# Performance work log

Measured on AMD Instinct MI355X. Metric: run time of the kernel, lower is better.

The kernel has to match this reference:

```python
import jax, jax.numpy as jnp
import numpy as np

N_FACES = 40000
N_EDGES = 60000
NNZ = 3 * N_FACES  # 3 boundary edges per triangular face
IN_CH = 512
MID_CH = 512
OUT_CH = 512


def setup_inputs() -> dict:
    key = jax.random.key(0)
    k1, k2, k3 = jax.random.split(key, 3)
    x = jax.random.normal(k1, (N_FACES, IN_CH), dtype=jnp.float32)
    # xavier-uniform-ish scale with gain 1.414 as in TopoModelX Conv.reset_parameters
    W1 = jax.random.normal(k2, (IN_CH, MID_CH), dtype=jnp.float32) * (1.414 / np.sqrt(IN_CH))
    W2 = jax.random.normal(k3, (MID_CH, OUT_CH), dtype=jnp.float32) * (1.414 / np.sqrt(MID_CH))
    # COO incidence B2 [n_edges, n_faces]: face f -> edges (3f)%E,(3f+1)%E,(3f+2)%E
    i = jnp.arange(NNZ)
    face_idx = (i // 3).astype(jnp.int32)
    edge_idx = (i % N_EDGES).astype(jnp.int32)
    vals = jnp.ones((NNZ,), dtype=jnp.float32)
    return {"x": x, "W1": W1, "W2": W2, "edge_idx": edge_idx, "face_idx": face_idx, "vals": vals}


def _spmm(rows, cols, vals, x, n_rows):
    # y[r, :] = sum_{nnz with row r} vals * x[col, :]
    return jax.ops.segment_sum(vals[:, None] * x[cols], rows, num_segments=n_rows)


def reference(x, W1, W2, edge_idx, face_idx, vals):
    # row sums of B2 and B2^T for aggr_norm
    deg_e = jax.ops.segment_sum(vals, edge_idx, num_segments=N_EDGES)  # [n_edges]
    deg_f = jax.ops.segment_sum(vals, face_idx, num_segments=N_FACES)  # [n_faces]
    # conv level1: faces -> edges
    h = _spmm(edge_idx, face_idx, vals, x @ W1, N_EDGES)  # [n_edges, mid]
    h = jax.nn.sigmoid(h / deg_e[:, None])
    # conv level2: edges -> faces (transpose incidence)
    y = _spmm(face_idx, edge_idx, vals, h @ W2, N_FACES)  # [n_faces, out]
    return jax.nn.sigmoid(y / deg_f[:, None])
```

## Files before the change

kernel.cpp:

```cpp
#include <hip/hip_runtime.h>
#include <cstdint>

#define N_FACES_C 40000
#define N_EDGES_C 60000
#define CH        512

typedef __bf16 bf16_t;
typedef __bf16 bf16x8 __attribute__((ext_vector_type(8)));
typedef float  f32x4  __attribute__((ext_vector_type(4)));
static_assert(sizeof(bf16x8) == 16, "bf16x8 must be 16B");

__global__ void detect_dtype(const unsigned int* __restrict__ vals_bits, int* __restrict__ flag) {
  if (blockIdx.x == 0 && threadIdx.x == 0)
    *flag = (vals_bits[0] == 0x3F803F80u) ? 1 : 0;
}

__device__ __forceinline__ float load_val(const void* vals, int i, bool isbf16) {
  return isbf16 ? (float)((const bf16_t*)vals)[i] : ((const float*)vals)[i];
}

__device__ __forceinline__ float fast_sigmoid(float z) {
  float e = __builtin_amdgcn_exp2f(z * -1.44269504f);
  return __builtin_amdgcn_rcpf(1.0f + e);
}

__device__ __forceinline__ void swz_block(int gx, int gy, int& obx, int& oby) {
  int orig = blockIdx.y * gx + blockIdx.x;
  int nwg = gx * gy;
  int q = nwg >> 3, r = nwg & 7;
  int xcd = orig & 7, idx = orig >> 3;
  int wg = (xcd < r ? xcd * (q + 1) : r * (q + 1) + (xcd - r) * q) + idx;
  obx = wg % gx;
  oby = wg / gx;
}

__global__ void count_deg_kernel(const int* __restrict__ ei, const int* __restrict__ fi,
                                 const void* __restrict__ vals, int nnz,
                                 float* __restrict__ deg_e, float* __restrict__ deg_f,
                                 int* __restrict__ cnt_e, int* __restrict__ cnt_f,
                                 const int* __restrict__ flag) {
  int i = blockIdx.x * 256 + threadIdx.x;
  if (i >= nnz) return;
  bool isb = (*flag != 0);
  float v = load_val(vals, i, isb);
  int e = ei[i], f = fi[i];
  atomicAdd(&deg_e[e], v);
  atomicAdd(&deg_f[f], v);
  atomicAdd(&cnt_e[e], 1);
  atomicAdd(&cnt_f[f], 1);
}

__global__ void scan_part2(const int* __restrict__ cntE, int nE, int* __restrict__ bsumE,
                           const int* __restrict__ cntF, int nF, int* __restrict__ bsumF,
                           int nbE) {
  __shared__ int wsum[4];
  int bx = blockIdx.x;
  const int* cnt; int n; int* bsum; int b;
  if (bx < nbE) { cnt = cntE; n = nE; bsum = bsumE; b = bx; }
  else          { cnt = cntF; n = nF; bsum = bsumF; b = bx - nbE; }
  int t = threadIdx.x;
  int lane = t & 63, wave = t >> 6;
  int base = b * 1024 + t * 4;
  int s = 0;
#pragma unroll
  for (int k = 0; k < 4; ++k) {
    int idx = base + k;
    if (idx < n) s += cnt[idx];
  }
#pragma unroll
  for (int o = 32; o > 0; o >>= 1) s += __shfl_down(s, o);
  if (lane == 0) wsum[wave] = s;
  __syncthreads();
  if (t == 0) bsum[b] = wsum[0] + wsum[1] + wsum[2] + wsum[3];
}

__global__ void scan_bsums2(int* __restrict__ bsumE, int nbE, int* __restrict__ bsumF, int nbF) {
  int wave = threadIdx.x >> 6;
  int lane = threadIdx.x & 63;
  int* bsum = wave ? bsumF : bsumE;
  int nb    = wave ? nbF   : nbE;
  int orig = (lane < nb) ? bsum[lane] : 0;
  int v = orig;
#pragma unroll
  for (int o = 1; o < 64; o <<= 1) {
    int u = __shfl_up(v, o);
    if (lane >= o) v += u;
  }
  if (lane < nb) bsum[lane] = v - orig;
}

__global__ void scan_final2(const int* __restrict__ cntE, int nE, const int* __restrict__ bsumE,
                            int* __restrict__ ptrE, int* __restrict__ curE,
                            const int* __restrict__ cntF, int nF, const int* __restrict__ bsumF,
                            int* __restrict__ ptrF, int* __restrict__ curF, int nbE) {
  __shared__ int wsum[4];
  int bx = blockIdx.x;
  const int* cnt; int n; const int* bsum; int* ptr; int* cur; int b;
  if (bx < nbE) { cnt = cntE; n = nE; bsum = bsumE; ptr = ptrE; cur = curE; b = bx; }
  else          { cnt = cntF; n = nF; bsum = bsumF; ptr = ptrF; cur = curF; b = bx - nbE; }
  int t = threadIdx.x;
  int lane = t & 63, wave = t >> 6;
  int base = b * 1024 + t * 4;
  int c[4];
  int s = 0;
#pragma unroll
  for (int k = 0; k < 4; ++k) {
    int idx = base + k;
    c[k] = (idx < n) ? cnt[idx] : 0;
    s += c[k];
  }
  int v = s;
#pragma unroll
  for (int o = 1; o < 64; o <<= 1) {
    int u = __shfl_up(v, o);
    if (lane >= o) v += u;
  }
  if (lane == 63) wsum[wave] = v;
  __syncthreads();
  int woff = 0;
  for (int w = 0; w < wave; ++w) woff += wsum[w];
  int run = bsum[b] + woff + (v - s);
#pragma unroll
  for (int k = 0; k < 4; ++k) {
    int idx = base + k;
    if (idx < n) {
      ptr[idx] = run;
      cur[idx] = run;
      run += c[k];
      if (idx == n - 1) ptr[n] = run;
    }
  }
}

__global__ void csr_fill(const int* __restrict__ ei, const int* __restrict__ fi,
                         const void* __restrict__ vals, int nnz,
                         int* __restrict__ cur_e, int* __restrict__ col_e, float* __restrict__ val_e,
                         int* __restrict__ cur_f, int* __restrict__ col_f, float* __restrict__ val_f,
                         const int* __restrict__ flag) {
  int i = blockIdx.x * 256 + threadIdx.x;
  if (i >= nnz) return;
  bool isb = (*flag != 0);
  int e = ei[i], f = fi[i];
  float v = load_val(vals, i, isb);
  int p = atomicAdd(&cur_e[e], 1);
  col_e[p] = f; val_e[p] = v;
  int q = atomicAdd(&cur_f[f], 1);
  col_f[q] = e; val_f[q] = v;
}

__global__ void transposeW2(const void* __restrict__ W1, bf16_t* __restrict__ W1t,
                            const void* __restrict__ W2, bf16_t* __restrict__ W2t,
                            const int* __restrict__ flag) {
  __shared__ bf16_t tile[32][33];
  bool isb = (*flag != 0);
  const void* W = blockIdx.z ? W2 : W1;
  bf16_t*    Wt = blockIdx.z ? W2t : W1t;
  int bx = blockIdx.x * 32, by = blockIdx.y * 32;
  int tx = threadIdx.x, ty = threadIdx.y;
#pragma unroll
  for (int r = 0; r < 32; r += 8) {
    size_t idx = (size_t)(by + ty + r) * CH + bx + tx;
    tile[ty + r][tx] = isb ? ((const bf16_t*)W)[idx] : (bf16_t)((const float*)W)[idx];
  }
  __syncthreads();
#pragma unroll
  for (int r = 0; r < 32; r += 8)
    Wt[(size_t)(bx + ty + r) * CH + by + tx] = tile[tx][ty + r];
}

template <int SIG>
__global__ void spmm_row(const int* __restrict__ ptr, const int* __restrict__ cols,
                         const float* __restrict__ vals, const bf16_t* __restrict__ X,
                         const float* __restrict__ deg, bf16_t* __restrict__ Y,
                         int nRows, int nCols, int nnz) {
  int row = blockIdx.x * 4 + (threadIdx.x >> 6);
  if (row >= nRows) return;
  int lane = threadIdx.x & 63;
  int beg = ptr[row], end = ptr[row + 1];
  if (beg < 0) beg = 0;
  if (end > nnz) end = nnz;
  float acc[8];
#pragma unroll
  for (int t = 0; t < 8; ++t) acc[t] = 0.f;
  const int lofs = lane * 8;
  for (int p = beg; p < end; ++p) {
    int c = cols[p];
    if ((unsigned)c >= (unsigned)nCols) c = 0;
    float v = vals[p];
    bf16x8 xv = *(const bf16x8*)(X + (size_t)c * CH + lofs);
#pragma unroll
    for (int t = 0; t < 8; ++t) acc[t] += v * (float)xv[t];
  }
  float d = deg[row];
  float invd = (d != 0.f) ? (1.0f / d) : 0.f;
  bf16x8 o;
#pragma unroll
  for (int t = 0; t < 8; ++t) {
    float z = acc[t] * invd;
    o[t] = (bf16_t)(SIG ? fast_sigmoid(z) : z);
  }
  *(bf16x8*)(Y + (size_t)row * CH + lofs) = o;
}

__global__ __launch_bounds__(256)
void gemm_xw(const void* __restrict__ A, const bf16_t* __restrict__ Bt,
             bf16_t* __restrict__ C, int M, const int* __restrict__ flag) {
  __shared__ __align__(16) bf16_t As[128 * 64];
  __shared__ __align__(16) bf16_t Bs[128 * 64];
  const int tid  = threadIdx.x;
  const int lane = tid & 63;
  const int wave = tid >> 6;
  int bx, by;
  swz_block(gridDim.x, gridDim.y, bx, by);
  const int r0 = by * 128;
  const int c0 = bx * 128;
  const int wr = (wave >> 1) * 64;
  const int wc = (wave & 1) * 64;
  const int q   = lane >> 4;
  const int l16 = lane & 15;
  const int srow_base = wave * 8 + (lane >> 3);
  const int sslot = lane & 7;
  const bool ab = (*flag != 0);

  f32x4 acc[4][4];
#pragma unroll
  for (int i = 0; i < 4; ++i)
#pragma unroll
    for (int j = 0; j < 4; ++j)
      acc[i][j] = (f32x4){0.f, 0.f, 0.f, 0.f};

  for (int kt = 0; kt < 8; ++kt) {
    const int kb = kt * 64;
    if (ab) {
      const bf16_t* Ab = (const bf16_t*)A;
#pragma unroll
      for (int i = 0; i < 4; ++i) {
        const int lr = i * 32 + srow_base;
        const int gofs = (sslot ^ (lr & 7)) * 8;
        int ra = r0 + lr; if (ra > M - 1) ra = M - 1;
        __builtin_amdgcn_global_load_lds((const __attribute__((address_space(1))) void*)(Ab + (size_t)ra * CH + kb + gofs),
                                         (__attribute__((address_space(3))) void*)(As + (i * 32 + wave * 8) * 64), 16, 0, 0);
        __builtin_amdgcn_global_load_lds((const __attribute__((address_space(1))) void*)(Bt + (size_t)(c0 + lr) * CH + kb + gofs),
                                         (__attribute__((address_space(3))) void*)(Bs + (i * 32 + wave * 8) * 64), 16, 0, 0);
      }
    } else {
      const float* Af = (const float*)A;
#pragma unroll
      for (int i = 0; i < 4; ++i) {
        const int lr = i * 32 + srow_base;
        const int gofs = (sslot ^ (lr & 7)) * 8;
        int ra = r0 + lr; if (ra > M - 1) ra = M - 1;
        const float* src = Af + (size_t)ra * CH + kb + gofs;
        float4 a = *(const float4*)src;
        float4 b = *(const float4*)(src + 4);
        bf16x8 v;
        v[0] = (bf16_t)a.x; v[1] = (bf16_t)a.y; v[2] = (bf16_t)a.z; v[3] = (bf16_t)a.w;
        v[4] = (bf16_t)b.x; v[5] = (bf16_t)b.y; v[6] = (bf16_t)b.z; v[7] = (bf16_t)b.w;
        *(bf16x8*)(As + lr * 64 + sslot * 8) = v;
        __builtin_amdgcn_global_load_lds((const __attribute__((address_space(1))) void*)(Bt + (size_t)(c0 + lr) * CH + kb + gofs),
                                         (__attribute__((address_space(3))) void*)(Bs + (i * 32 + wave * 8) * 64), 16, 0, 0);
      }
    }
    __syncthreads();

#pragma unroll
    for (int kk = 0; kk < 2; ++kk) {
      const int slot = (kk * 4 + q) ^ (l16 & 7);
      const int ro = slot * 8;
      bf16x8 af[4], bfv[4];
#pragma unroll
      for (int i = 0; i < 4; ++i)
        af[i] = *(const bf16x8*)(As + (wr + i * 16 + l16) * 64 + ro);
#pragma unroll
      for (int j = 0; j < 4; ++j)
        bfv[j] = *(const bf16x8*)(Bs + (wc + j * 16 + l16) * 64 + ro);
#pragma unroll
      for (int i = 0; i < 4; ++i)
#pragma unroll
        for (int j = 0; j < 4; ++j)
          acc[i][j] = __builtin_amdgcn_mfma_f32_16x16x32_bf16(af[i], bfv[j], acc[i][j], 0, 0, 0);
    }
    __syncthreads();
  }

#pragma unroll
  for (int i = 0; i < 4; ++i) {
#pragma unroll
    for (int r = 0; r < 4; ++r) {
      int row = r0 + wr + i * 16 + q * 4 + r;
      if (row < M) {
#pragma unroll
        for (int j = 0; j < 4; ++j) {
          int col = c0 + wc + j * 16 + l16;
          C[(size_t)row * CH + col] = (bf16_t)acc[i][j][r];
        }
      }
    }
  }
}

__global__ __launch_bounds__(256)
void gemm_sig(const bf16_t* __restrict__ A, const bf16_t* __restrict__ Bt,
              void* __restrict__ C, int M,
              const int* __restrict__ flag) {
  __shared__ __align__(16) bf16_t As[128 * 64];
  __shared__ __align__(16) bf16_t Bs[128 * 64];
  const int tid  = threadIdx.x;
  const int lane = tid & 63;
  const int wave = tid >> 6;
  int bx, by;
  swz_block(gridDim.x, gridDim.y, bx, by);
  const int r0 = by * 128;
  const int c0 = bx * 128;
  const int wr = (wave >> 1) * 64;
  const int wc = (wave & 1) * 64;
  const int q   = lane >> 4;
  const int l16 = lane & 15;
  const int srow_base = wave * 8 + (lane >> 3);
  const int sslot = lane & 7;

  f32x4 acc[4][4];
#pragma unroll
  for (int i = 0; i < 4; ++i)
#pragma unroll
    for (int j = 0; j < 4; ++j)
      acc[i][j] = (f32x4){0.f, 0.f, 0.f, 0.f};

  for (int kt = 0; kt < 8; ++kt) {
    const int kb = kt * 64;
#pragma unroll
    for (int i = 0; i < 4; ++i) {
      const int lr = i * 32 + srow_base;
      const int gofs = (sslot ^ (lr & 7)) * 8;
      int ra = r0 + lr; if (ra > M - 1) ra = M - 1;
      const bf16_t* ga = A  + (size_t)ra * CH + kb + gofs;
      const bf16_t* gb = Bt + (size_t)(c0 + lr) * CH + kb + gofs;
      __builtin_amdgcn_global_load_lds((const __attribute__((address_space(1))) void*)ga,
                                       (__attribute__((address_space(3))) void*)(As + (i * 32 + wave * 8) * 64), 16, 0, 0);
      __builtin_amdgcn_global_load_lds((const __attribute__((address_space(1))) void*)gb,
                                       (__attribute__((address_space(3))) void*)(Bs + (i * 32 + wave * 8) * 64), 16, 0, 0);
    }
    __syncthreads();

#pragma unroll
    for (int kk = 0; kk < 2; ++kk) {
      const int slot = (kk * 4 + q) ^ (l16 & 7);
      const int ro = slot * 8;
      bf16x8 af[4], bfv[4];
#pragma unroll
      for (int i = 0; i < 4; ++i)
        af[i] = *(const bf16x8*)(As + (wr + i * 16 + l16) * 64 + ro);
#pragma unroll
      for (int j = 0; j < 4; ++j)
        bfv[j] = *(const bf16x8*)(Bs + (wc + j * 16 + l16) * 64 + ro);
#pragma unroll
      for (int i = 0; i < 4; ++i)
#pragma unroll
        for (int j = 0; j < 4; ++j)
          acc[i][j] = __builtin_amdgcn_mfma_f32_16x16x32_bf16(af[i], bfv[j], acc[i][j], 0, 0, 0);
    }
    __syncthreads();
  }

  const bool f32out = (*flag == 0);
#pragma unroll
  for (int i = 0; i < 4; ++i) {
#pragma unroll
    for (int r = 0; r < 4; ++r) {
      int row = r0 + wr + i * 16 + q * 4 + r;
      if (row < M) {
#pragma unroll
        for (int j = 0; j < 4; ++j) {
          int col = c0 + wc + j * 16 + l16;
          float s = fast_sigmoid(acc[i][j][r]);
          if (f32out) ((float*)C)[(size_t)row * CH + col] = s;
          else        ((bf16_t*)C)[(size_t)row * CH + col] = (bf16_t)s;
        }
      }
    }
  }
}

extern "C" void kernel_launch(void* const* d_in, const int* in_sizes, int n_in,
                              void* d_out, int out_size, void* d_ws, size_t ws_size,
                              hipStream_t stream) {
  const void* x    = d_in[0];
  const void* W1   = d_in[1];
  const void* W2   = d_in[2];
  const int*  ei   = (const int*)d_in[3];
  const int*  fi   = (const int*)d_in[4];
  const void* vals = d_in[5];
  const int nnz = in_sizes[3];

  char* ws = (char*)d_ws;
  size_t off = 0;
  auto alloc = [&](size_t bytes) -> void* {
    void* p = ws + off;
    off = (off + bytes + 511) & ~((size_t)511);
    return p;
  };
  bf16_t* t    = (bf16_t*)alloc((size_t)N_FACES_C * CH * 2);
  bf16_t* h    = (bf16_t*)alloc((size_t)N_EDGES_C * CH * 2);
  bf16_t* g    = (bf16_t*)alloc((size_t)N_FACES_C * CH * 2);
  bf16_t* w1t  = (bf16_t*)alloc((size_t)CH * CH * 2);
  bf16_t* w2t  = (bf16_t*)alloc((size_t)CH * CH * 2);
  float* deg_e = (float*)alloc((size_t)N_EDGES_C * 4);
  float* deg_f = (float*)alloc((size_t)N_FACES_C * 4);
  int*   cnt_e = (int*)alloc((size_t)N_EDGES_C * 4);
  int*   cnt_f = (int*)alloc((size_t)N_FACES_C * 4);
  size_t zero_bytes = (size_t)((char*)cnt_f + (size_t)N_FACES_C * 4 - (char*)deg_e);
  int*   ptr_e = (int*)alloc((size_t)(N_EDGES_C + 1) * 4);
  int*   ptr_f = (int*)alloc((size_t)(N_FACES_C + 1) * 4);
  int*   cur_e = (int*)alloc((size_t)N_EDGES_C * 4);
  int*   cur_f = (int*)alloc((size_t)N_FACES_C * 4);
  int*   col_e = (int*)alloc((size_t)nnz * 4);
  float* val_e = (float*)alloc((size_t)nnz * 4);
  int*   col_f = (int*)alloc((size_t)nnz * 4);
  float* val_f = (float*)alloc((size_t)nnz * 4);
  int*   bsumE = (int*)alloc(64 * 4);
  int*   bsumF = (int*)alloc(64 * 4);
  int*   flag  = (int*)alloc(4);

  detect_dtype<<<1, 64, 0, stream>>>((const unsigned int*)vals, flag);
  hipMemsetAsync(deg_e, 0, zero_bytes, stream);
  count_deg_kernel<<<(nnz + 255) / 256, 256, 0, stream>>>(ei, fi, vals, nnz,
                                                          deg_e, deg_f, cnt_e, cnt_f, flag);

  int nbE = (N_EDGES_C + 1023) / 1024, nbF = (N_FACES_C + 1023) / 1024;
  scan_part2 <<<nbE + nbF, 256, 0, stream>>>(cnt_e, N_EDGES_C, bsumE, cnt_f, N_FACES_C, bsumF, nbE);
  scan_bsums2<<<1, 128, 0, stream>>>(bsumE, nbE, bsumF, nbF);
  scan_final2<<<nbE + nbF, 256, 0, stream>>>(cnt_e, N_EDGES_C, bsumE, ptr_e, cur_e,
                                             cnt_f, N_FACES_C, bsumF, ptr_f, cur_f, nbE);
  csr_fill<<<(nnz + 255) / 256, 256, 0, stream>>>(ei, fi, vals, nnz,
                                                  cur_e, col_e, val_e, cur_f, col_f, val_f, flag);

  transposeW2<<<dim3(16, 16, 2), dim3(32, 8), 0, stream>>>(W1, w1t, W2, w2t, flag);

  gemm_xw<<<dim3(CH / 128, (N_FACES_C + 127) / 128), 256, 0, stream>>>(x, w1t, t, N_FACES_C, flag);
  spmm_row<1><<<(N_EDGES_C + 3) / 4, 256, 0, stream>>>(ptr_e, col_e, val_e, t, deg_e, h,
                                                       N_EDGES_C, N_FACES_C, nnz);
  spmm_row<0><<<(N_FACES_C + 3) / 4, 256, 0, stream>>>(ptr_f, col_f, val_f, h, deg_f, g,
                                                       N_FACES_C, N_EDGES_C, nnz);
  gemm_sig<<<dim3(CH / 128, (N_FACES_C + 127) / 128), 256, 0, stream>>>(g, w2t, d_out,
                                                                        N_FACES_C, flag);
}
```

Measured before the change: 315.0 us.

## Double-buffer LDS tiles in both GEMM kernels to overlap loads with MFMA

Both GEMM kernels now keep two LDS buffers per operand and prefetch the next K-tile while MFMAs run on the current one. One barrier per iteration replaces the previous two. The fp32 input path holds the next tile in registers and converts and stores it after compute. The aim is to hide global-load latency behind matrix math, at the cost of doubled LDS use (64KB per block), which may lower occupancy.

New measurement: 311.3 us. No clear change (-1.2%).

```diff
diff --git a/kernel.cpp b/kernel.cpp
--- a/kernel.cpp
+++ b/kernel.cpp
@@ -202,11 +202,12 @@
   *(bf16x8*)(Y + (size_t)row * CH + lofs) = o;
 }
 
+
 __global__ __launch_bounds__(256)
 void gemm_xw(const void* __restrict__ A, const bf16_t* __restrict__ Bt,
              bf16_t* __restrict__ C, int M, const int* __restrict__ flag) {
-  __shared__ __align__(16) bf16_t As[128 * 64];
-  __shared__ __align__(16) bf16_t Bs[128 * 64];
+  __shared__ __align__(16) bf16_t As[2][128 * 64];
+  __shared__ __align__(16) bf16_t Bs[2][128 * 64];
   const int tid  = threadIdx.x;
   const int lane = tid & 63;
   const int wave = tid >> 6;
@@ -222,6 +223,15 @@
   const int sslot = lane & 7;
   const bool ab = (*flag != 0);
 
+  int lr_[4], gofs_[4], ra_[4];
+#pragma unroll
+  for (int i = 0; i < 4; ++i) {
+    lr_[i] = i * 32 + srow_base;
+    gofs_[i] = (sslot ^ (lr_[i] & 7)) * 8;
+    int ra = r0 + lr_[i]; if (ra > M - 1) ra = M - 1;
+    ra_[i] = ra;
+  }
+
   f32x4 acc[4][4];
 #pragma unroll
   for (int i = 0; i < 4; ++i)
@@ -229,40 +239,62 @@
     for (int j = 0; j < 4; ++j)
       acc[i][j] = (f32x4){0.f, 0.f, 0.f, 0.f};
 
+  if (ab) {
+    const bf16_t* Ab = (const bf16_t*)A;
+#pragma unroll
+    for (int i = 0; i < 4; ++i) {
+      __builtin_amdgcn_global_load_lds((const __attribute__((address_space(1))) void*)(Ab + (size_t)ra_[i] * CH + gofs_[i]),
+                                       (__attribute__((address_space(3))) void*)(As[0] + (i * 32 + wave * 8) * 64), 16, 0, 0);
+      __builtin_amdgcn_global_load_lds((const __attribute__((address_space(1))) void*)(Bt + (size_t)(c0 + lr_[i]) * CH + gofs_[i]),
+                                       (__attribute__((address_space(3))) void*)(Bs[0] + (i * 32 + wave * 8) * 64), 16, 0, 0);
+    }
+  } else {
+    const float* Af = (const float*)A;
+#pragma unroll
+    for (int i = 0; i < 4; ++i) {
+      const float* src = Af + (size_t)ra_[i] * CH + gofs_[i];
+      float4 a = *(const float4*)src;
+      float4 b = *(const float4*)(src + 4);
+      bf16x8 v;
+      v[0] = (bf16_t)a.x; v[1] = (bf16_t)a.y; v[2] = (bf16_t)a.z; v[3] = (bf16_t)a.w;
+      v[4] = (bf16_t)b.x; v[5] = (bf16_t)b.y; v[6] = (bf16_t)b.z; v[7] = (bf16_t)b.w;
+      *(bf16x8*)(As[0] + lr_[i] * 64 + sslot * 8) = v;
+      __builtin_amdgcn_global_load_lds((const __attribute__((address_space(1))) void*)(Bt + (size_t)(c0 + lr_[i]) * CH + gofs_[i]),
+                                       (__attribute__((address_space(3))) void*)(Bs[0] + (i * 32 + wave * 8) * 64), 16, 0, 0);
+    }
+  }
+  __syncthreads();
+
+  int cur = 0;
   for (int kt = 0; kt < 8; ++kt) {
-    const int kb = kt * 64;
-    if (ab) {
-      const bf16_t* Ab = (const bf16_t*)A;
-#pragma unroll
-      for (int i = 0; i < 4; ++i) {
-        const int lr = i * 32 + srow_base;
-        const int gofs = (sslot ^ (lr & 7)) * 8;
-        int ra = r0 + lr; if (ra > M - 1) ra = M - 1;
-        __builtin_amdgcn_global_load_lds((const __attribute__((address_space(1))) void*)(Ab + (size_t)ra * CH + kb + gofs),
-                                         (__attribute__((address_space(3))) void*)(As + (i * 32 + wave * 8) * 64), 16, 0, 0);
-        __builtin_amdgcn_global_load_lds((const __attribute__((address_space(1))) void*)(Bt + (size_t)(c0 + lr) * CH + kb + gofs),
-                                         (__attribute__((address_space(3))) void*)(Bs + (i * 32 + wave * 8) * 64), 16, 0, 0);
+    const int nb = cur ^ 1;
+    const bool has_next = (kt < 7);
+    float4 pa[4], pb[4];
+    if (has_next) {
+      const int kb = (kt + 1) * 64;
+      if (ab) {
+        const bf16_t* Ab = (const bf16_t*)A;
+#pragma unroll
+        for (int i = 0; i < 4; ++i) {
+          __builtin_amdgcn_global_load_lds((const __attribute__((address_space(1))) void*)(Ab + (size_t)ra_[i] * CH + kb + gofs_[i]),
+                                           (__attribute__((address_space(3))) void*)(As[nb] + (i * 32 + wave * 8) * 64), 16, 0, 0);
+          __builtin_amdgcn_global_load_lds((const __attribute__((address_space(1))) void*)(Bt + (size_t)(c0 + lr_[i]) * CH + kb + gofs_[i]),
+                                           (__attribute__((address_space(3))) void*)(Bs[nb] + (i * 32 + wave * 8) * 64), 16, 0, 0);
+        }
+      } else {
+        const float* Af = (const float*)A;
+#pragma unroll
+        for (int i = 0; i < 4; ++i) {
+          const float* src = Af + (size_t)ra_[i] * CH + kb + gofs_[i];
+          pa[i] = *(const float4*)src;
+          pb[i] = *(const float4*)(src + 4);
+        }
+#pragma unroll
+        for (int i = 0; i < 4; ++i)
+          __builtin_amdgcn_global_load_lds((const __attribute__((address_space(1))) void*)(Bt + (size_t)(c0 + lr_[i]) * CH + kb + gofs_[i]),
+                                           (__attribute__((address_space(3))) void*)(Bs[nb] + (i * 32 + wave * 8) * 64), 16, 0, 0);
       }
-    } else {
-      const float* Af = (const float*)A;
-#pragma unroll
-      for (int i = 0; i < 4; ++i) {
-        const int lr = i * 32 + srow_base;
-        const int gofs = (sslot ^ (lr & 7)) * 8;
-        int ra = r0 + lr; if (ra > M - 1) ra = M - 1;
-        const float* src = Af + (size_t)ra * CH + kb + gofs;
-        float4 a = *(const float4*)src;
-        float4 b = *(const float4*)(src + 4);
-        bf16x8 v;
-        v[0] = (bf16_t)a.x; v[1] = (bf16_t)a.y; v[2] = (bf16_t)a.z; v[3] = (bf16_t)a.w;
-        v[4] = (bf16_t)b.x; v[5] = (bf16_t)b.y; v[6] = (bf16_t)b.z; v[7] = (bf16_t)b.w;
-        *(bf16x8*)(As + lr * 64 + sslot * 8) = v;
-        __builtin_amdgcn_global_load_lds((const __attribute__((address_space(1))) void*)(Bt + (size_t)(c0 + lr) * CH + kb + gofs),
-                                         (__attribute__((address_space(3))) void*)(Bs + (i * 32 + wave * 8) * 64), 16, 0, 0);
-      }
-    }
-    __syncthreads();
-
+    }
 #pragma unroll
     for (int kk = 0; kk < 2; ++kk) {
       const int slot = (kk * 4 + q) ^ (l16 & 7);
@@ -270,17 +302,27 @@
       bf16x8 af[4], bfv[4];
 #pragma unroll
       for (int i = 0; i < 4; ++i)
-        af[i] = *(const bf16x8*)(As + (wr + i * 16 + l16) * 64 + ro);
+        af[i] = *(const bf16x8*)(As[cur] + (wr + i * 16 + l16) * 64 + ro);
 #pragma unroll
       for (int j = 0; j < 4; ++j)
-        bfv[j] = *(const bf16x8*)(Bs + (wc + j * 16 + l16) * 64 + ro);
+        bfv[j] = *(const bf16x8*)(Bs[cur] + (wc + j * 16 + l16) * 64 + ro);
 #pragma unroll
       for (int i = 0; i < 4; ++i)
 #pragma unroll
         for (int j = 0; j < 4; ++j)
           acc[i][j] = __builtin_amdgcn_mfma_f32_16x16x32_bf16(af[i], bfv[j], acc[i][j], 0, 0, 0);
     }
+    if (has_next && !ab) {
+#pragma unroll
+      for (int i = 0; i < 4; ++i) {
+        bf16x8 v;
+        v[0] = (bf16_t)pa[i].x; v[1] = (bf16_t)pa[i].y; v[2] = (bf16_t)pa[i].z; v[3] = (bf16_t)pa[i].w;
+        v[4] = (bf16_t)pb[i].x; v[5] = (bf16_t)pb[i].y; v[6] = (bf16_t)pb[i].z; v[7] = (bf16_t)pb[i].w;
+        *(bf16x8*)(As[nb] + lr_[i] * 64 + sslot * 8) = v;
+      }
+    }
     __syncthreads();
+    cur = nb;
   }
 
 #pragma unroll
@@ -301,10 +343,9 @@
 
 __global__ __launch_bounds__(256)
 void gemm_sig(const bf16_t* __restrict__ A, const bf16_t* __restrict__ Bt,
-              void* __restrict__ C, int M,
-              const int* __restrict__ flag) {
-  __shared__ __align__(16) bf16_t As[128 * 64];
-  __shared__ __align__(16) bf16_t Bs[128 * 64];
+              void* __restrict__ C, int M, const int* __restrict__ flag) {
+  __shared__ __align__(16) bf16_t As[2][128 * 64];
+  __shared__ __align__(16) bf16_t Bs[2][128 * 64];
   const int tid  = threadIdx.x;
   const int lane = tid & 63;
   const int wave = tid >> 6;
@@ -319,6 +360,15 @@
   const int srow_base = wave * 8 + (lane >> 3);
   const int sslot = lane & 7;
 
+  int lr_[4], gofs_[4], ra_[4];
+#pragma unroll
+  for (int i = 0; i < 4; ++i) {
+    lr_[i] = i * 32 + srow_base;
+    gofs_[i] = (sslot ^ (lr_[i] & 7)) * 8;
+    int ra = r0 + lr_[i]; if (ra > M - 1) ra = M - 1;
+    ra_[i] = ra;
+  }
+
   f32x4 acc[4][4];
 #pragma unroll
   for (int i = 0; i < 4; ++i)
@@ -326,22 +376,28 @@
     for (int j = 0; j < 4; ++j)
       acc[i][j] = (f32x4){0.f, 0.f, 0.f, 0.f};
 
+#pragma unroll
+  for (int i = 0; i < 4; ++i) {
+    __builtin_amdgcn_global_load_lds((const __attribute__((address_space(1))) void*)(A + (size_t)ra_[i] * CH + gofs_[i]),
+                                     (__attribute__((address_space(3))) void*)(As[0] + (i * 32 + wave * 8) * 64), 16, 0, 0);
+    __builtin_amdgcn_global_load_lds((const __attribute__((address_space(1))) void*)(Bt + (size_t)(c0 + lr_[i]) * CH + gofs_[i]),
+                                     (__attribute__((address_space(3))) void*)(Bs[0] + (i * 32 + wave * 8) * 64), 16, 0, 0);
+  }
+  __syncthreads();
+
+  int cur = 0;
   for (int kt = 0; kt < 8; ++kt) {
-    const int kb = kt * 64;
-#pragma unroll
-    for (int i = 0; i < 4; ++i) {
-      const int lr = i * 32 + srow_base;
-      const int gofs = (sslot ^ (lr & 7)) * 8;
-      int ra = r0 + lr; if (ra > M - 1) ra = M - 1;
-      const bf16_t* ga = A  + (size_t)ra * CH + kb + gofs;
-      const bf16_t* gb = Bt + (size_t)(c0 + lr) * CH + kb + gofs;
-      __builtin_amdgcn_global_load_lds((const __attribute__((address_space(1))) void*)ga,
-                                       (__attribute__((address_space(3))) void*)(As + (i * 32 + wave * 8) * 64), 16, 0, 0);
-      __builtin_amdgcn_global_load_lds((const __attribute__((address_space(1))) void*)gb,
-                                       (__attribute__((address_space(3))) void*)(Bs + (i * 32 + wave * 8) * 64), 16, 0, 0);
-    }
-    __syncthreads();
-
+    const int nb = cur ^ 1;
+    if (kt < 7) {
+      const int kb = (kt + 1) * 64;
+#pragma unroll
+      for (int i = 0; i < 4; ++i) {
+        __builtin_amdgcn_global_load_lds((const __attribute__((address_space(1))) void*)(A + (size_t)ra_[i] * CH + kb + gofs_[i]),
+                                         (__attribute__((address_space(3))) void*)(As[nb] + (i * 32 + wave * 8) * 64), 16, 0, 0);
+        __builtin_amdgcn_global_load_lds((const __attribute__((address_space(1))) void*)(Bt + (size_t)(c0 + lr_[i]) * CH + kb + gofs_[i]),
+                                         (__attribute__((address_space(3))) void*)(Bs[nb] + (i * 32 + wave * 8) * 64), 16, 0, 0);
+      }
+    }
 #pragma unroll
     for (int kk = 0; kk < 2; ++kk) {
       const int slot = (kk * 4 + q) ^ (l16 & 7);
@@ -349,10 +405,10 @@
       bf16x8 af[4], bfv[4];
 #pragma unroll
       for (int i = 0; i < 4; ++i)
-        af[i] = *(const bf16x8*)(As + (wr + i * 16 + l16) * 64 + ro);
+        af[i] = *(const bf16x8*)(As[cur] + (wr + i * 16 + l16) * 64 + ro);
 #pragma unroll
       for (int j = 0; j < 4; ++j)
-        bfv[j] = *(const bf16x8*)(Bs + (wc + j * 16 + l16) * 64 + ro);
+        bfv[j] = *(const bf16x8*)(Bs[cur] + (wc + j * 16 + l16) * 64 + ro);
 #pragma unroll
       for (int i = 0; i < 4; ++i)
 #pragma unroll
@@ -360,6 +416,7 @@
           acc[i][j] = __builtin_amdgcn_mfma_f32_16x16x32_bf16(af[i], bfv[j], acc[i][j], 0, 0, 0);
     }
     __syncthreads();
+    cur = nb;
   }
 
   const bool f32out = (*flag == 0);
```
